# Kernel tuning notes

Measured on AMD Instinct MI355X. Metric: run time of the kernel, lower is better.

Reference implementation:

```python
import jax, jax.numpy as jnp
import numpy as np

BETA = 0.25


def setup_inputs() -> dict:
    key = jax.random.key(0)
    k1, k2 = jax.random.split(key)
    x = jax.random.normal(k1, (32, 512, 32, 32), dtype=jnp.float32)
    # torchhd Random embedding: random bipolar {-1,+1} hypervectors, non-trainable
    codebook = jnp.sign(jax.random.normal(k2, (1024, 512), dtype=jnp.float32))
    codebook = jnp.where(codebook == 0, 1.0, codebook)
    return {"x": x, "codebook": codebook}


def reference(x, codebook):
    B, C, W, H = x.shape
    K = codebook.shape[0]
    # training-mode path: sharp sigmoid soft-binarization -> [-1, 1]
    xs = jax.nn.sigmoid(x * 100.0) * 2.0 - 1.0
    # [B, C, W, H] -> [B*W*H, C]
    flat = jnp.transpose(xs, (0, 2, 3, 1)).reshape(-1, C)
    # squared-distance via norms + matmul (same expansion as the torch code)
    d = (
        jnp.sum(flat * flat, axis=1, keepdims=True)
        + jnp.sum(codebook * codebook, axis=1)
        - 2.0 * flat @ codebook.T
    )  # [N, K]
    indices = jnp.argmin(d, axis=1)  # [N]
    # perplexity from empirical code usage (unique+counts == bincount over present codes)
    counts = jnp.bincount(indices, length=K).astype(jnp.float32)
    n = jnp.asarray(indices.shape[0], dtype=jnp.float32)
    p = counts / n
    plogp = jnp.where(counts > 0, p * jnp.log(p), 0.0)
    entropy = -jnp.sum(plogp)
    perplexity = jnp.exp(entropy)
    perplexity_loss = 1.0 / perplexity
    loss = BETA * perplexity_loss
    # embedding gather + reshape back to [B, C, W, H]
    q = codebook[indices].reshape(B, W, H, C)
    q = jnp.transpose(q, (0, 3, 1, 2))
    # straight-through estimator
    quantized = xs + jax.lax.stop_gradient(q - xs)
    return quantized, perplexity_loss, loss
```

## Files before the change

kernel.cpp:

```cpp
#include <hip/hip_runtime.h>
#include <stdint.h>
#include <stddef.h>

#define CD 512
#define KC 1024
#define NR 32768

typedef __attribute__((ext_vector_type(8))) short short8_t;
typedef __attribute__((ext_vector_type(8))) __bf16 bf16x8_t;
typedef __attribute__((ext_vector_type(4))) float f32x4_t;

__device__ __forceinline__ uint16_t f2bf(float f) {
  uint32_t u = __float_as_uint(f);
  u += 0x7fffu + ((u >> 16) & 1u);
  return (uint16_t)(u >> 16);
}
__device__ __forceinline__ float bf2f(uint16_t h) {
  return __uint_as_float(((uint32_t)h) << 16);
}
__device__ __forceinline__ float soft_sign(float x) {
  float e = __expf(-100.0f * x);
  float s = __builtin_amdgcn_rcpf(1.0f + e);
  return fmaf(2.0f, s, -1.0f);
}

__global__ __launch_bounds__(256) void k_cb(const float* __restrict__ cb,
                                            uint16_t* __restrict__ cbb,
                                            uint32_t* __restrict__ pack) {
  int i = blockIdx.x * 256 + threadIdx.x;
  float v = cb[i];
  cbb[i] = f2bf(v);
  int k = i >> 9, c = i & 511;
  unsigned long long m = __ballot(v > 0.0f);
  int lane = threadIdx.x & 63;
  if ((lane & 31) == 0) pack[((c >> 5) << 10) + k] = (uint32_t)(m >> (lane & 32));
}

__device__ __forceinline__ void gl_lds16(const uint16_t* g, uint16_t* l) {
  __builtin_amdgcn_global_load_lds((const uint32_t*)g, (uint32_t*)l, 16, 0, 0);
}

__global__ __launch_bounds__(512, 1) void k_gemm(const uint16_t* __restrict__ cbb,
                                                 const float* __restrict__ x,
                                                 int* __restrict__ idx,
                                                 int* __restrict__ counts) {
  extern __shared__ uint8_t smem[];
  uint16_t* lds = (uint16_t*)smem;

  const int tid = threadIdx.x;
  const int lane = tid & 63, wid = tid >> 6;
  const int kg = wid >> 1, pg = wid & 1;
  const int g = lane >> 4, r15 = lane & 15;
  const int blk = blockIdx.x;
  const int n0 = blk << 6;
  const int b = blk >> 4, p0 = (blk & 15) << 6;

  auto stageA = [&](int buf, int kt, int cc) {
    uint16_t* dst = lds + (buf << 13);
    const uint16_t* srcb = cbb + ((size_t)(kt << 8)) * 512 + (cc << 5);
#pragma unroll
    for (int i = 0; i < 2; ++i) {
      int u = (i << 9) + tid;
      gl_lds16(srcb + (size_t)(u >> 2) * 512 + ((u & 3) << 3), dst + (u << 3));
    }
  };
  stageA(0, 0, 0);

  float* raw = (float*)(smem + 16384);
  const float* xb = x + (((size_t)b) << 19) + p0;
  const int fr = tid >> 3, foc = tid & 7;
  double nsum = 0.0;
  for (int ch = 0; ch < 8; ++ch) {
    int c0 = ch << 6;
#pragma unroll
    for (int it = 0; it < 2; ++it) {
      int u = (it << 9) + tid;
      int cr = u >> 4, q = u & 15;
      const float4 v =
          *reinterpret_cast<const float4*>(xb + (size_t)(c0 + cr) * 1024 + (q << 2));
      *reinterpret_cast<float4*>(raw + (cr << 6) +
                                 ((q << 2) ^ ((((cr >> 3) & 7)) << 2))) = v;
    }
    __syncthreads();
    short8_t h8, l8;
    double ls = 0.0;
#pragma unroll
    for (int j = 0; j < 8; ++j) {
      int c = (foc << 3) + j;
      float xs = soft_sign(raw[(c << 6) + (fr ^ (foc << 2))]);
      uint16_t h = f2bf(xs);
      uint16_t l = f2bf(xs - bf2f(h));
      h8[j] = (short)h;
      l8[j] = (short)l;
      float sq = xs * xs;
      ls += (double)sq;
    }
    nsum += ls;
    int cc = (ch << 1) + (foc >> 2), jj = foc & 3;
    uint16_t* bwp = (uint16_t*)(smem + 32768 + (cc << 12)) + (fr << 5) + (jj << 3);
    *reinterpret_cast<short8_t*>(bwp) = h8;
    *reinterpret_cast<short8_t*>(bwp + 32768) = l8;
    __syncthreads();
  }
  {
    double s = nsum;
    s += __shfl_xor(s, 1);
    s += __shfl_xor(s, 2);
    s += __shfl_xor(s, 4);
    if (foc == 0) ((float*)raw)[fr] = (float)s + 512.0f;
  }
  __syncthreads();
  float s_p[2];
#pragma unroll
  for (int ac = 0; ac < 2; ++ac) s_p[ac] = ((float*)raw)[(pg << 5) + (ac << 4) + r15];
  __syncthreads();

  float best_d[2];
  int best_k[2];
#pragma unroll
  for (int ac = 0; ac < 2; ++ac) { best_d[ac] = 3.4e38f; best_k[ac] = 0; }

  f32x4_t acc[4][2];
  int cur = 0;
  for (int step = 0; step < 64; ++step) {
    int kt = step >> 4, cc = step & 15;
    if (cc == 0) {
#pragma unroll
      for (int i = 0; i < 4; ++i)
#pragma unroll
        for (int j = 0; j < 2; ++j) acc[i][j] = (f32x4_t){0.f, 0.f, 0.f, 0.f};
    }
    if (step < 63) {
      int ns = step + 1;
      stageA(cur ^ 1, ns >> 4, ns & 15);
    }

    const uint16_t* A = lds + (cur << 13);
    const uint16_t* Bh = (uint16_t*)(smem + 32768) + (cc << 11);
    bf16x8_t af[4], fbh[2], fbl[2];
#pragma unroll
    for (int ar = 0; ar < 4; ++ar) {
      int row = (kg << 6) + (ar << 4) + r15;
      af[ar] = __builtin_bit_cast(bf16x8_t,
                                  *(const short8_t*)(A + (row << 5) + (g << 3)));
    }
#pragma unroll
    for (int ac = 0; ac < 2; ++ac) {
      int row = (pg << 5) + (ac << 4) + r15;
      fbh[ac] = __builtin_bit_cast(bf16x8_t,
                                   *(const short8_t*)(Bh + (row << 5) + (g << 3)));
      fbl[ac] = __builtin_bit_cast(
          bf16x8_t, *(const short8_t*)(Bh + 32768 + (row << 5) + (g << 3)));
    }
#pragma unroll
    for (int ar = 0; ar < 4; ++ar)
#pragma unroll
      for (int ac = 0; ac < 2; ++ac) {
        acc[ar][ac] =
            __builtin_amdgcn_mfma_f32_16x16x32_bf16(af[ar], fbh[ac], acc[ar][ac], 0, 0, 0);
        acc[ar][ac] =
            __builtin_amdgcn_mfma_f32_16x16x32_bf16(af[ar], fbl[ac], acc[ar][ac], 0, 0, 0);
      }

    if (cc == 15) {
      int kbase = (kt << 8) + (kg << 6);
#pragma unroll
      for (int ar = 0; ar < 4; ++ar)
#pragma unroll
        for (int ac = 0; ac < 2; ++ac)
#pragma unroll
          for (int rg = 0; rg < 4; ++rg) {
            float d = fmaf(-2.0f, acc[ar][ac][rg], s_p[ac]);
            int kk = kbase + (ar << 4) + (g << 2) + rg;
            bool better = (d < best_d[ac]) || (d == best_d[ac] && kk < best_k[ac]);
            if (better) { best_d[ac] = d; best_k[ac] = kk; }
          }
    }

    asm volatile("s_waitcnt vmcnt(0)" ::: "memory");
    __builtin_amdgcn_s_barrier();
    asm volatile("" ::: "memory");
    cur ^= 1;
  }

  float rd0, rd1;
  int rk0, rk1;
  {
    float d = best_d[0];
    int k = best_k[0];
#pragma unroll
    for (int m = 16; m <= 32; m <<= 1) {
      float od = __shfl_xor(d, m);
      int ok = __shfl_xor(k, m);
      if (od < d || (od == d && ok < k)) { d = od; k = ok; }
    }
    rd0 = d; rk0 = k;
  }
  {
    float d = best_d[1];
    int k = best_k[1];
#pragma unroll
    for (int m = 16; m <= 32; m <<= 1) {
      float od = __shfl_xor(d, m);
      int ok = __shfl_xor(k, m);
      if (od < d || (od == d && ok < k)) { d = od; k = ok; }
    }
    rd1 = d; rk1 = k;
  }
  float* sd = (float*)smem;
  int* sk = (int*)(smem + 1024);
  __syncthreads();
  if (g < 2) {
    float dv = (g == 0) ? rd0 : rd1;
    int kv = (g == 0) ? rk0 : rk1;
    sd[(kg << 6) + (pg << 5) + (g << 4) + r15] = dv;
    sk[(kg << 6) + (pg << 5) + (g << 4) + r15] = kv;
  }
  __syncthreads();
  if (tid < 64) {
    float d0 = sd[tid];
    int k0 = sk[tid];
#pragma unroll
    for (int kgi = 1; kgi < 4; ++kgi) {
      float d1 = sd[(kgi << 6) + tid];
      int k1 = sk[(kgi << 6) + tid];
      if (d1 < d0 || (d1 == d0 && k1 < k0)) { d0 = d1; k0 = k1; }
    }
    idx[n0 + tid] = k0;
    atomicAdd(&counts[k0], 1);
  }
}

__global__ __launch_bounds__(256) void k_perp(const int* __restrict__ counts,
                                              float* __restrict__ out2) {
  int tid = threadIdx.x;
  float local = 0.0f;
  for (int i = tid; i < KC; i += 256) {
    int c = counts[i];
    if (c > 0) {
      float p = (float)c * (1.0f / 32768.0f);
      local += p * logf(p);
    }
  }
#pragma unroll
  for (int m = 1; m < 64; m <<= 1) local += __shfl_xor(local, m);
  __shared__ float wsum[4];
  if ((tid & 63) == 0) wsum[tid >> 6] = local;
  __syncthreads();
  if (tid == 0) {
    float entropy = -(wsum[0] + wsum[1] + wsum[2] + wsum[3]);
    float pl = 1.0f / expf(entropy);
    out2[0] = pl;
    out2[1] = 0.25f * pl;
  }
}

__global__ __launch_bounds__(256) void k_gather(const int* __restrict__ idx,
                                                const uint32_t* __restrict__ pack,
                                                float* __restrict__ out) {
  __shared__ uint32_t lp[16384];
  int tid = threadIdx.x;
#pragma unroll
  for (int i = 0; i < 16; ++i)
    reinterpret_cast<uint4*>(lp)[i * 256 + tid] =
        reinterpret_cast<const uint4*>(pack)[i * 256 + tid];
  __syncthreads();
  int base = blockIdx.x * 2048;
  for (int it = 0; it < 8; ++it) {
    int t = base + it * 256 + tid;
    int pq = t & 255;
    int c = (t >> 8) & 511;
    int b = t >> 17;
    int4 iv = reinterpret_cast<const int4*>(idx)[(b << 8) + pq];
    int cw = c >> 5, cbit = c & 31;
    float4 r;
    r.x = ((lp[(cw << 10) + iv.x] >> cbit) & 1) ? 1.0f : -1.0f;
    r.y = ((lp[(cw << 10) + iv.y] >> cbit) & 1) ? 1.0f : -1.0f;
    r.z = ((lp[(cw << 10) + iv.z] >> cbit) & 1) ? 1.0f : -1.0f;
    r.w = ((lp[(cw << 10) + iv.w] >> cbit) & 1) ? 1.0f : -1.0f;
    reinterpret_cast<float4*>(out)[t] = r;
  }
}

extern "C" void kernel_launch(void* const* d_in, const int* in_sizes, int n_in,
                              void* d_out, int out_size, void* d_ws, size_t ws_size,
                              hipStream_t stream) {
  (void)in_sizes; (void)n_in; (void)out_size; (void)ws_size;
  const float* x = (const float*)d_in[0];
  const float* cb = (const float*)d_in[1];
  float* out = (float*)d_out;

  uint8_t* ws = (uint8_t*)d_ws;
  uint16_t* cbb = (uint16_t*)ws;
  int* idx = (int*)(ws + 1048576);
  int* counts = (int*)(ws + 1048576 + 131072);
  uint32_t* pack = (uint32_t*)(ws + 1048576 + 131072 + 4096);

  hipFuncSetAttribute((const void*)k_gemm, hipFuncAttributeMaxDynamicSharedMemorySize,
                      163840);

  k_cb<<<2048, 256, 0, stream>>>(cb, cbb, pack);
  hipMemsetAsync(counts, 0, 4096, stream);
  k_gemm<<<512, 512, 163840, stream>>>(cbb, x, idx, counts);
  k_perp<<<1, 256, 0, stream>>>(counts, out + 16777216);
  k_gather<<<2048, 256, 0, stream>>>(idx, pack, out);
}
```

Baseline: 213.9 us.

## Deepen codebook pipeline to 4 stages, swizzle LDS, fuse memset and perplexity kernels

The GEMM main loop now streams 128-row codebook slices through a 4-deep LDS ring with vmcnt(2) waits, in place of 256-row double buffering with full drains. Each wave keeps fewer accumulators (2x2 instead of 4x2) and the loop runs 128 steps. XOR swizzles are added to the A and B LDS layouts to reduce bank conflicts. The counts memset is folded into k_cb and the perplexity kernel into block 0 of k_gather, removing two launches at the cost of more barriers per unit of MFMA work.

New measurement: 217.1 us. Within noise of the previous version (+1.5%).

```diff
diff --git a/kernel.cpp b/kernel.cpp
--- a/kernel.cpp
+++ b/kernel.cpp
@@ -26,7 +26,8 @@
 
 __global__ __launch_bounds__(256) void k_cb(const float* __restrict__ cb,
                                             uint16_t* __restrict__ cbb,
-                                            uint32_t* __restrict__ pack) {
+                                            uint32_t* __restrict__ pack,
+                                            int* __restrict__ counts) {
   int i = blockIdx.x * 256 + threadIdx.x;
   float v = cb[i];
   cbb[i] = f2bf(v);
@@ -34,6 +35,7 @@
   unsigned long long m = __ballot(v > 0.0f);
   int lane = threadIdx.x & 63;
   if ((lane & 31) == 0) pack[((c >> 5) << 10) + k] = (uint32_t)(m >> (lane & 32));
+  if (i < KC) counts[i] = 0;
 }
 
 __device__ __forceinline__ void gl_lds16(const uint16_t* g, uint16_t* l) {
@@ -55,18 +57,15 @@
   const int n0 = blk << 6;
   const int b = blk >> 4, p0 = (blk & 15) << 6;
 
-  auto stageA = [&](int buf, int kt, int cc) {
-    uint16_t* dst = lds + (buf << 13);
-    const uint16_t* srcb = cbb + ((size_t)(kt << 8)) * 512 + (cc << 5);
-#pragma unroll
-    for (int i = 0; i < 2; ++i) {
-      int u = (i << 9) + tid;
-      gl_lds16(srcb + (size_t)(u >> 2) * 512 + ((u & 3) << 3), dst + (u << 3));
-    }
+  const int srow_t = tid >> 2;
+  const int sg_t = (tid & 3) ^ ((tid >> 3) & 3);
+  const uint16_t* sbase = cbb + ((size_t)srow_t << 9) + (sg_t << 3);
+  auto stageA = [&](int u) {
+    gl_lds16(sbase + ((size_t)(u >> 4) << 16) + ((u & 15) << 5),
+             lds + ((u & 3) << 12) + (tid << 3));
   };
-  stageA(0, 0, 0);
-
-  float* raw = (float*)(smem + 16384);
+
+  float* raw = (float*)smem;
   const float* xb = x + (((size_t)b) << 19) + p0;
   const int fr = tid >> 3, foc = tid & 7;
   double nsum = 0.0;
@@ -96,8 +95,9 @@
       ls += (double)sq;
     }
     nsum += ls;
-    int cc = (ch << 1) + (foc >> 2), jj = foc & 3;
-    uint16_t* bwp = (uint16_t*)(smem + 32768 + (cc << 12)) + (fr << 5) + (jj << 3);
+    int cc = (ch << 1) + (foc >> 2);
+    int gp = (foc & 3) ^ ((fr >> 1) & 3);
+    uint16_t* bwp = (uint16_t*)(smem + 32768) + (cc << 11) + (fr << 5) + (gp << 3);
     *reinterpret_cast<short8_t*>(bwp) = h8;
     *reinterpret_cast<short8_t*>(bwp + 32768) = l8;
     __syncthreads();
@@ -107,53 +107,64 @@
     s += __shfl_xor(s, 1);
     s += __shfl_xor(s, 2);
     s += __shfl_xor(s, 4);
-    if (foc == 0) ((float*)raw)[fr] = (float)s + 512.0f;
+    if (foc == 0) raw[fr] = (float)s + 512.0f;
   }
   __syncthreads();
   float s_p[2];
 #pragma unroll
-  for (int ac = 0; ac < 2; ++ac) s_p[ac] = ((float*)raw)[(pg << 5) + (ac << 4) + r15];
-  __syncthreads();
+  for (int ac = 0; ac < 2; ++ac) s_p[ac] = raw[(pg << 5) + (ac << 4) + r15];
+  __syncthreads();
+
+  int offA[2], offB[2];
+#pragma unroll
+  for (int ar = 0; ar < 2; ++ar) {
+    int row = (kg << 5) + (ar << 4) + r15;
+    offA[ar] = (row << 5) + ((g ^ ((row >> 1) & 3)) << 3);
+  }
+#pragma unroll
+  for (int ac = 0; ac < 2; ++ac) {
+    int row = (pg << 5) + (ac << 4) + r15;
+    offB[ac] = (row << 5) + ((g ^ ((row >> 1) & 3)) << 3);
+  }
+
+  stageA(0);
+  stageA(1);
+  stageA(2);
 
   float best_d[2];
   int best_k[2];
 #pragma unroll
   for (int ac = 0; ac < 2; ++ac) { best_d[ac] = 3.4e38f; best_k[ac] = 0; }
 
-  f32x4_t acc[4][2];
-  int cur = 0;
-  for (int step = 0; step < 64; ++step) {
-    int kt = step >> 4, cc = step & 15;
+  f32x4_t acc[2][2];
+  for (int s = 0; s < 128; ++s) {
+    int kt = s >> 4, cc = s & 15;
+    asm volatile("s_waitcnt vmcnt(2)" ::: "memory");
+    __builtin_amdgcn_s_barrier();
+    asm volatile("" ::: "memory");
+    stageA((s + 3) & 127);
+
     if (cc == 0) {
 #pragma unroll
-      for (int i = 0; i < 4; ++i)
+      for (int i = 0; i < 2; ++i)
 #pragma unroll
         for (int j = 0; j < 2; ++j) acc[i][j] = (f32x4_t){0.f, 0.f, 0.f, 0.f};
     }
-    if (step < 63) {
-      int ns = step + 1;
-      stageA(cur ^ 1, ns >> 4, ns & 15);
-    }
-
-    const uint16_t* A = lds + (cur << 13);
+
+    const uint16_t* A = lds + ((s & 3) << 12);
     const uint16_t* Bh = (uint16_t*)(smem + 32768) + (cc << 11);
-    bf16x8_t af[4], fbh[2], fbl[2];
-#pragma unroll
-    for (int ar = 0; ar < 4; ++ar) {
-      int row = (kg << 6) + (ar << 4) + r15;
-      af[ar] = __builtin_bit_cast(bf16x8_t,
-                                  *(const short8_t*)(A + (row << 5) + (g << 3)));
-    }
+    bf16x8_t af[2], fbh[2], fbl[2];
+#pragma unroll
+    for (int ar = 0; ar < 2; ++ar)
+      af[ar] = __builtin_bit_cast(bf16x8_t, *(const short8_t*)(A + offA[ar]));
 #pragma unroll
     for (int ac = 0; ac < 2; ++ac) {
-      int row = (pg << 5) + (ac << 4) + r15;
-      fbh[ac] = __builtin_bit_cast(bf16x8_t,
-                                   *(const short8_t*)(Bh + (row << 5) + (g << 3)));
-      fbl[ac] = __builtin_bit_cast(
-          bf16x8_t, *(const short8_t*)(Bh + 32768 + (row << 5) + (g << 3)));
-    }
-#pragma unroll
-    for (int ar = 0; ar < 4; ++ar)
+      fbh[ac] = __builtin_bit_cast(bf16x8_t, *(const short8_t*)(Bh + offB[ac]));
+      fbl[ac] =
+          __builtin_bit_cast(bf16x8_t, *(const short8_t*)(Bh + 32768 + offB[ac]));
+    }
+#pragma unroll
+    for (int ar = 0; ar < 2; ++ar)
 #pragma unroll
       for (int ac = 0; ac < 2; ++ac) {
         acc[ar][ac] =
@@ -163,9 +174,9 @@
       }
 
     if (cc == 15) {
-      int kbase = (kt << 8) + (kg << 6);
-#pragma unroll
-      for (int ar = 0; ar < 4; ++ar)
+      int kbase = (kt << 7) + (kg << 5);
+#pragma unroll
+      for (int ar = 0; ar < 2; ++ar)
 #pragma unroll
         for (int ac = 0; ac < 2; ++ac)
 #pragma unroll
@@ -176,11 +187,6 @@
             if (better) { best_d[ac] = d; best_k[ac] = kk; }
           }
     }
-
-    asm volatile("s_waitcnt vmcnt(0)" ::: "memory");
-    __builtin_amdgcn_s_barrier();
-    asm volatile("" ::: "memory");
-    cur ^= 1;
   }
 
   float rd0, rd1;
@@ -207,6 +213,7 @@
     }
     rd1 = d; rk1 = k;
   }
+  asm volatile("s_waitcnt vmcnt(0)" ::: "memory");
   float* sd = (float*)smem;
   int* sk = (int*)(smem + 1024);
   __syncthreads();
@@ -231,35 +238,33 @@
   }
 }
 
-__global__ __launch_bounds__(256) void k_perp(const int* __restrict__ counts,
-                                              float* __restrict__ out2) {
-  int tid = threadIdx.x;
-  float local = 0.0f;
-  for (int i = tid; i < KC; i += 256) {
-    int c = counts[i];
-    if (c > 0) {
-      float p = (float)c * (1.0f / 32768.0f);
-      local += p * logf(p);
-    }
-  }
-#pragma unroll
-  for (int m = 1; m < 64; m <<= 1) local += __shfl_xor(local, m);
-  __shared__ float wsum[4];
-  if ((tid & 63) == 0) wsum[tid >> 6] = local;
-  __syncthreads();
-  if (tid == 0) {
-    float entropy = -(wsum[0] + wsum[1] + wsum[2] + wsum[3]);
-    float pl = 1.0f / expf(entropy);
-    out2[0] = pl;
-    out2[1] = 0.25f * pl;
-  }
-}
-
 __global__ __launch_bounds__(256) void k_gather(const int* __restrict__ idx,
                                                 const uint32_t* __restrict__ pack,
+                                                const int* __restrict__ counts,
                                                 float* __restrict__ out) {
   __shared__ uint32_t lp[16384];
   int tid = threadIdx.x;
+  if (blockIdx.x == 0) {
+    float local = 0.0f;
+    for (int i = tid; i < KC; i += 256) {
+      int c = counts[i];
+      if (c > 0) {
+        float p = (float)c * (1.0f / 32768.0f);
+        local += p * logf(p);
+      }
+    }
+#pragma unroll
+    for (int m = 1; m < 64; m <<= 1) local += __shfl_xor(local, m);
+    __shared__ float wsum[4];
+    if ((tid & 63) == 0) wsum[tid >> 6] = local;
+    __syncthreads();
+    if (tid == 0) {
+      float entropy = -(wsum[0] + wsum[1] + wsum[2] + wsum[3]);
+      float pl = 1.0f / expf(entropy);
+      out[16777216] = pl;
+      out[16777217] = 0.25f * pl;
+    }
+  }
 #pragma unroll
   for (int i = 0; i < 16; ++i)
     reinterpret_cast<uint4*>(lp)[i * 256 + tid] =
@@ -299,9 +304,7 @@
   hipFuncSetAttribute((const void*)k_gemm, hipFuncAttributeMaxDynamicSharedMemorySize,
                       163840);
 
-  k_cb<<<2048, 256, 0, stream>>>(cb, cbb, pack);
-  hipMemsetAsync(counts, 0, 4096, stream);
+  k_cb<<<2048, 256, 0, stream>>>(cb, cbb, pack, counts);
   k_gemm<<<512, 512, 163840, stream>>>(cbb, x, idx, counts);
-  k_perp<<<1, 256, 0, stream>>>(counts, out + 16777216);
-  k_gather<<<2048, 256, 0, stream>>>(idx, pack, out);
-}
+  k_gather<<<2048, 256, 0, stream>>>(idx, pack, counts, out);
+}
```
